# Kernel tuning notes

Measured on AMD Instinct MI355X. Metric: run time of the kernel, lower is better.

The kernel has to match this reference:

```python
import jax, jax.numpy as jnp
import numpy as np

_EPS = 1e-6

def _qmul(q1, q2):  # xyzw quaternion product
    x1, y1, z1, w1 = q1[..., 0], q1[..., 1], q1[..., 2], q1[..., 3]
    x2, y2, z2, w2 = q2[..., 0], q2[..., 1], q2[..., 2], q2[..., 3]
    return jnp.stack([
        w1 * x2 + x1 * w2 + y1 * z2 - z1 * y2,
        w1 * y2 + y1 * w2 + z1 * x2 - x1 * z2,
        w1 * z2 + z1 * w2 + x1 * y2 - y1 * x2,
        w1 * w2 - x1 * x2 - y1 * y2 - z1 * z2], axis=-1)

def _qrot(q, v):  # rotate v by unit quaternion q (xyzw)
    qv, qw = q[..., :3], q[..., 3:4]
    t = 2.0 * jnp.cross(qv, v)
    return v + qw * t + jnp.cross(qv, t)

def _so3_log(q):  # quaternion (xyzw) -> rotation vector phi
    qv, qw = q[..., :3], q[..., 3:4]
    n2 = jnp.sum(qv * qv, axis=-1, keepdims=True)
    small = n2 < _EPS * _EPS
    n = jnp.sqrt(jnp.where(small, 1.0, n2))
    factor = jnp.where(small,
                       2.0 / qw - (2.0 / 3.0) * n2 / qw ** 3,
                       2.0 * jnp.arctan2(n, qw) / n)
    return factor * qv

def _so3_exp(phi):  # rotation vector -> quaternion (xyzw)
    t2 = jnp.sum(phi * phi, axis=-1, keepdims=True)
    small = t2 < _EPS * _EPS
    theta = jnp.sqrt(jnp.where(small, 1.0, t2))
    half = 0.5 * theta
    s = jnp.where(small, 0.5 - t2 / 48.0, jnp.sin(half) / theta)
    w = jnp.where(small, 1.0 - t2 / 8.0, jnp.cos(half))
    return jnp.concatenate([s * phi, w], axis=-1)

def _jl(phi, v):  # SO3 left Jacobian J_l(phi) @ v
    t2 = jnp.sum(phi * phi, axis=-1, keepdims=True)
    small = t2 < _EPS * _EPS
    t2s = jnp.where(small, 1.0, t2)
    theta = jnp.sqrt(t2s)
    a = jnp.where(small, 0.5 - t2 / 24.0, (1.0 - jnp.cos(theta)) / t2s)
    b = jnp.where(small, 1.0 / 6.0 - t2 / 120.0, (theta - jnp.sin(theta)) / (t2s * theta))
    c1 = jnp.cross(phi, v)
    return v + a * c1 + b * jnp.cross(phi, c1)

def _jl_inv(phi, v):  # SO3 left Jacobian inverse J_l^{-1}(phi) @ v
    t2 = jnp.sum(phi * phi, axis=-1, keepdims=True)
    small = t2 < _EPS * _EPS
    t2s = jnp.where(small, 1.0, t2)
    theta = jnp.sqrt(t2s)
    s = jnp.sin(theta)
    s_safe = jnp.where(jnp.abs(s) < _EPS, _EPS, s)
    c = jnp.where(small, 1.0 / 12.0 + t2 / 720.0,
                  1.0 / t2s - (1.0 + jnp.cos(theta)) / (2.0 * theta * s_safe))
    c1 = jnp.cross(phi, v)
    return v - 0.5 * c1 + c * jnp.cross(phi, c1)

def _se3_inv(T):
    t, q = T[..., :3], T[..., 3:]
    qi = q * jnp.array([-1.0, -1.0, -1.0, 1.0], dtype=T.dtype)
    return jnp.concatenate([-_qrot(qi, t), qi], axis=-1)

def _se3_mul(T1, T2):
    t1, q1 = T1[..., :3], T1[..., 3:]
    t2, q2 = T2[..., :3], T2[..., 3:]
    return jnp.concatenate([t1 + _qrot(q1, t2), _qmul(q1, q2)], axis=-1)

def _se3_log(T):  # SE3 -> se3 [tau, phi]
    t, q = T[..., :3], T[..., 3:]
    phi = _so3_log(q)
    return jnp.concatenate([_jl_inv(phi, t), phi], axis=-1)

def _se3_exp(xi):  # se3 [tau, phi] -> SE3
    tau, phi = xi[..., :3], xi[..., 3:]
    q = _so3_exp(phi)
    return jnp.concatenate([_jl(phi, tau), q], axis=-1)

def _forward(input_poses, time):
    # duplicate first/last pose (inter_begin_and_end=True)
    poses = jnp.concatenate([input_poses[:, :1], input_poses, input_poses[:, -1:]], axis=1)
    B, P = poses.shape[0], poses.shape[1]
    S = P - 3  # number of spline segments
    u = time.reshape(-1)  # [K]
    K = u.shape[0]
    U = jnp.stack([jnp.ones_like(u), u, u * u, u * u * u], axis=0)  # [4,K]
    M = jnp.array([[5., 3., -3., 1.], [1., 3., 3., -2.], [0., 0., 0., 1.]], dtype=u.dtype) / 6.0
    w = M @ U  # [3,K] cumulative B-spline weights
    p0, p1 = poses[:, 0:S], poses[:, 1:S + 1]
    p2, p3 = poses[:, 2:S + 2], poses[:, 3:S + 3]
    d0 = _se3_log(_se3_mul(_se3_inv(p0), p1))  # [B,S,6]
    d1 = _se3_log(_se3_mul(_se3_inv(p1), p2))
    d2 = _se3_log(_se3_mul(_se3_inv(p2), p3))
    A0 = _se3_exp(d0[:, :, None, :] * w[0][None, None, :, None])  # [B,S,K,7]
    A1 = _se3_exp(d1[:, :, None, :] * w[1][None, None, :, None])
    A2 = _se3_exp(d2[:, :, None, :] * w[2][None, None, :, None])
    Td = jnp.broadcast_to(p0[:, :, None, :], (B, S, K, 7))
    out = _se3_mul(_se3_mul(_se3_mul(Td, A0), A1), A2)
    return out.reshape(B, S * K, 7)

def setup_inputs() -> dict:
    key = jax.random.key(0)
    k1, k2, k3 = jax.random.split(key, 3)
    B, N, K = 32, 2048, 32
    t = jax.random.normal(k1, (B, N, 3), dtype=jnp.float32) * 2.0
    q = jax.random.normal(k2, (B, N, 4), dtype=jnp.float32)
    q = q / jnp.linalg.norm(q, axis=-1, keepdims=True)
    q = jnp.where(q[..., 3:4] < 0, -q, q)  # qw >= 0 for well-conditioned Log
    input_poses = jnp.concatenate([t, q], axis=-1)
    time = jax.random.uniform(k3, (1, 1, K), dtype=jnp.float32)
    return {"input_poses": input_poses, "time": time}

def reference(input_poses, time):
    return _forward(input_poses, time)
```

## Files before the change

### kernel.cpp

```cpp
#include <hip/hip_runtime.h>
#include <cmath>

namespace {

constexpr int BATCH  = 32;
constexpr int NPOSE  = 2048;
constexpr int KSAMP  = 32;
constexpr int NSEG   = NPOSE - 1;
constexpr int NDELTA = NPOSE + 1;
constexpr int SEGB   = 32;
constexpr float EPS  = 1e-6f;
constexpr float EPS2 = 1e-12f;
constexpr float INV_TWO_PI = 0.15915494309189535f;

struct V3 { float x, y, z; };
struct Q4 { float x, y, z, w; };
struct SE3 { V3 t; Q4 q; };

__device__ __forceinline__ float frcp(float x)  { return __builtin_amdgcn_rcpf(x); }
__device__ __forceinline__ float fsqrt(float x) { return __builtin_amdgcn_sqrtf(x); }
__device__ __forceinline__ float fsin(float x)  { return __builtin_amdgcn_sinf(x * INV_TWO_PI); }
__device__ __forceinline__ float fcos(float x)  { return __builtin_amdgcn_cosf(x * INV_TWO_PI); }

__device__ __forceinline__ V3 v3add(V3 a, V3 b) { return {a.x + b.x, a.y + b.y, a.z + b.z}; }
__device__ __forceinline__ V3 v3sub(V3 a, V3 b) { return {a.x - b.x, a.y - b.y, a.z - b.z}; }
__device__ __forceinline__ V3 v3scl(V3 a, float s) { return {a.x * s, a.y * s, a.z * s}; }
__device__ __forceinline__ float v3dot(V3 a, V3 b) { return a.x * b.x + a.y * b.y + a.z * b.z; }
__device__ __forceinline__ V3 v3cross(V3 a, V3 b) {
    return {a.y * b.z - a.z * b.y, a.z * b.x - a.x * b.z, a.x * b.y - a.y * b.x};
}

__device__ __forceinline__ V3 qrot(Q4 q, V3 v) {
    V3 qv{q.x, q.y, q.z};
    V3 t = v3scl(v3cross(qv, v), 2.0f);
    return v3add(v3add(v, v3scl(t, q.w)), v3cross(qv, t));
}

__device__ __forceinline__ Q4 qmul(Q4 a, Q4 b) {
    return {a.w * b.x + a.x * b.w + a.y * b.z - a.z * b.y,
            a.w * b.y + a.y * b.w + a.z * b.x - a.x * b.z,
            a.w * b.z + a.z * b.w + a.x * b.y - a.y * b.x,
            a.w * b.w - a.x * b.x - a.y * b.y - a.z * b.z};
}

__device__ __forceinline__ SE3 se3_mul(SE3 A, SE3 Bv) {
    SE3 r;
    r.t = v3add(A.t, qrot(A.q, Bv.t));
    r.q = qmul(A.q, Bv.q);
    return r;
}

__device__ __forceinline__ float facos(float x) {
    float ax = fabsf(x);
    float p = -0.0012624911f;
    p = p * ax + 0.0066700901f;
    p = p * ax - 0.0170881256f;
    p = p * ax + 0.0308918810f;
    p = p * ax - 0.0501743046f;
    p = p * ax + 0.0889789874f;
    p = p * ax - 0.2145988016f;
    p = p * ax + 1.5707963050f;
    float r = fsqrt(fmaxf(1.0f - ax, 0.0f)) * p;
    return (x >= 0.0f) ? r : (3.14159265358979f - r);
}

__device__ __forceinline__ V3 so3_log(Q4 q) {
    V3 qv{q.x, q.y, q.z};
    float n2 = v3dot(qv, qv);
    bool small = n2 < EPS2;
    float n = fsqrt(small ? 1.0f : n2);
    float iw = frcp(q.w);
    float f_small = 2.0f * iw - (2.0f / 3.0f) * n2 * iw * iw * iw;
    float wc = fminf(fmaxf(q.w, -1.0f), 1.0f);
    float f_big = 2.0f * facos(wc) * frcp(n);
    return v3scl(qv, small ? f_small : f_big);
}

__device__ __forceinline__ V3 jl_inv(V3 phi, V3 v) {
    float t2 = v3dot(phi, phi);
    bool small = t2 < EPS2;
    float t2s = small ? 1.0f : t2;
    float theta = fsqrt(t2s);
    float s = fsin(theta), cth = fcos(theta);
    float s_safe = (fabsf(s) < EPS) ? EPS : s;
    float c_big = frcp(t2s) - (1.0f + cth) * frcp(2.0f * theta * s_safe);
    float c = small ? (1.0f / 12.0f + t2 * (1.0f / 720.0f)) : c_big;
    V3 c1 = v3cross(phi, v);
    return v3add(v3sub(v, v3scl(c1, 0.5f)), v3scl(v3cross(phi, c1), c));
}

__global__ __launch_bounds__(256) void lie_delta_kernel(
    const float* __restrict__ poses,
    float4* __restrict__ ws)
{
    const int i = blockIdx.x * 256 + threadIdx.x;
    const int b = blockIdx.y;
    if (i >= NDELTA) return;

    int ia = max(i - 1, 0);
    int ib = min(i, NPOSE - 1);
    const float* Pa = poses + ((size_t)b * NPOSE + ia) * 7;
    const float* Pb = poses + ((size_t)b * NPOSE + ib) * 7;
    V3 ta{Pa[0], Pa[1], Pa[2]}; Q4 qa{Pa[3], Pa[4], Pa[5], Pa[6]};
    V3 tb{Pb[0], Pb[1], Pb[2]}; Q4 qb{Pb[3], Pb[4], Pb[5], Pb[6]};

    Q4 qi{-qa.x, -qa.y, -qa.z, qa.w};
    V3 trel = qrot(qi, v3sub(tb, ta));
    Q4 qrel = qmul(qi, qb);
    V3 phi = so3_log(qrel);
    V3 tau = jl_inv(phi, trel);

    float n2 = v3dot(phi, phi);
    float nphi = fsqrt(n2);
    float inv_n = frcp(fmaxf(nphi, 1e-20f));
    V3 u  = v3scl(phi, inv_n);
    V3 c1 = v3cross(u, tau);
    V3 c2 = v3cross(u, c1);

    float4* row = ws + ((size_t)b * NDELTA + i) * 4;
    row[0] = make_float4(tau.x, tau.y, tau.z, nphi);
    row[1] = make_float4(u.x,  u.y,  u.z,  0.0f);
    row[2] = make_float4(c1.x, c1.y, c1.z, 0.0f);
    row[3] = make_float4(c2.x, c2.y, c2.z, 0.0f);
}

__device__ __forceinline__ SE3 exp_fast(float4 A, float4 U, float4 C1, float4 C2, float w) {
    float th = fmaxf(w * A.w, 1e-12f);
    float sh = fsin(0.5f * th), ch = fcos(0.5f * th);
    float it = frcp(th);
    float sA = 2.0f * sh * sh * it;
    float sB = 1.0f - 2.0f * sh * ch * it;
    SE3 r;
    r.q = {sh * U.x, sh * U.y, sh * U.z, ch};
    r.t = {w * (A.x + sA * C1.x + sB * C2.x),
           w * (A.y + sA * C1.y + sB * C2.y),
           w * (A.z + sA * C1.z + sB * C2.z)};
    return r;
}

__global__ __launch_bounds__(256) void lie_spline_kernel(
    const float* __restrict__ poses,
    const float* __restrict__ timev,
    const float4* __restrict__ ws,
    float* __restrict__ out)
{
    __shared__ float4 sdel[(SEGB + 2) * 5];
    __shared__ __align__(16) float stage[SEGB * KSAMP * 7];

    const int b   = blockIdx.y;
    const int s0  = blockIdx.x * SEGB;
    const int tid = threadIdx.x;

    if (tid < (SEGB + 2) * 4) {
        int row = tid >> 2, r = tid & 3;
        int idx = min(s0 + row, NDELTA - 1);
        sdel[row * 5 + r] = ws[((size_t)b * NDELTA + idx) * 4 + r];
    }

    const int segl = tid >> 3;
    const int s    = s0 + segl;
    const int m    = tid & 7;

    int ip = min(max(s - 1, 0), NPOSE - 1);
    const float* P0 = poses + ((size_t)b * NPOSE + ip) * 7;
    const SE3 Tp{{P0[0], P0[1], P0[2]}, {P0[3], P0[4], P0[5], P0[6]}};
    float4 uvec = reinterpret_cast<const float4*>(timev)[m];

    __syncthreads();

    const float4* R = sdel + segl * 5;
    float4 A0 = R[0],  U0 = R[1],  C10 = R[2],  C20 = R[3];
    float4 A1 = R[5],  U1 = R[6],  C11 = R[7],  C21 = R[8];
    float4 A2 = R[10], U2 = R[11], C12 = R[12], C22 = R[13];

    __align__(16) float buf[28];
    const float us[4] = {uvec.x, uvec.y, uvec.z, uvec.w};
    #pragma unroll
    for (int j = 0; j < 4; ++j) {
        float u  = us[j];
        float u2 = u * u, u3 = u2 * u;
        const float c6 = 1.0f / 6.0f;
        float w0 = (5.0f + 3.0f * u - 3.0f * u2 + u3) * c6;
        float w1 = (1.0f + 3.0f * u + 3.0f * u2 - 2.0f * u3) * c6;
        float w2 = u3 * c6;
        SE3 T = se3_mul(Tp, exp_fast(A0, U0, C10, C20, w0));
        T = se3_mul(T, exp_fast(A1, U1, C11, C21, w1));
        T = se3_mul(T, exp_fast(A2, U2, C12, C22, w2));
        float* d = buf + j * 7;
        d[0] = T.t.x; d[1] = T.t.y; d[2] = T.t.z;
        d[3] = T.q.x; d[4] = T.q.y; d[5] = T.q.z; d[6] = T.q.w;
    }

    if (s < NSEG) {
        float4* sv = reinterpret_cast<float4*>(stage + segl * (KSAMP * 7) + m * 28);
        const float4* bv = reinterpret_cast<const float4*>(buf);
        #pragma unroll
        for (int c = 0; c < 7; ++c) sv[c] = bv[c];
    }
    __syncthreads();

    int nseg_blk = min(NSEG - s0, SEGB);
    int nvec = nseg_blk * (KSAMP * 7 / 4);
    const float4* svv = reinterpret_cast<const float4*>(stage);
    float4* ov = reinterpret_cast<float4*>(out + ((size_t)b * NSEG + s0) * (size_t)(KSAMP * 7));
    for (int j = tid; j < nvec; j += 256) ov[j] = svv[j];
}

}

extern "C" void kernel_launch(void* const* d_in, const int* in_sizes, int n_in,
                              void* d_out, int out_size, void* d_ws, size_t ws_size,
                              hipStream_t stream) {
    const float* poses = (const float*)d_in[0];
    const float* timev = (const float*)d_in[1];
    float* out = (float*)d_out;
    float4* ws = (float4*)d_ws;
    (void)in_sizes; (void)n_in; (void)out_size; (void)ws_size;

    dim3 g1((NDELTA + 255) / 256, BATCH);
    lie_delta_kernel<<<g1, 256, 0, stream>>>(poses, ws);

    dim3 g2((NSEG + SEGB - 1) / SEGB, BATCH);
    lie_spline_kernel<<<g2, 256, 0, stream>>>(poses, timev, ws, out);
}
```

Measured before the change: 90.02 us.

## Fuse delta computation into spline kernel, computing deltas in shared memory per block

Removes the separate delta kernel and its global workspace round trip. Each spline block now computes its 34 needed deltas (SE3 log plus precomputed cross terms) directly into shared memory, with the first 34 threads doing the work before the barrier. It also skips pose evaluation for out-of-range segments and writes the staged poses straight from registers instead of through a private buffer. In exchange, one launch is saved, but each block recomputes two boundary deltas and serializes the transcendental-heavy delta work on a subset of threads before the barrier.

```diff
diff --git a/kernel.cpp b/kernel.cpp
--- a/kernel.cpp
+++ b/kernel.cpp
@@ -89,41 +89,6 @@
     return v3add(v3sub(v, v3scl(c1, 0.5f)), v3scl(v3cross(phi, c1), c));
 }
 
-__global__ __launch_bounds__(256) void lie_delta_kernel(
-    const float* __restrict__ poses,
-    float4* __restrict__ ws)
-{
-    const int i = blockIdx.x * 256 + threadIdx.x;
-    const int b = blockIdx.y;
-    if (i >= NDELTA) return;
-
-    int ia = max(i - 1, 0);
-    int ib = min(i, NPOSE - 1);
-    const float* Pa = poses + ((size_t)b * NPOSE + ia) * 7;
-    const float* Pb = poses + ((size_t)b * NPOSE + ib) * 7;
-    V3 ta{Pa[0], Pa[1], Pa[2]}; Q4 qa{Pa[3], Pa[4], Pa[5], Pa[6]};
-    V3 tb{Pb[0], Pb[1], Pb[2]}; Q4 qb{Pb[3], Pb[4], Pb[5], Pb[6]};
-
-    Q4 qi{-qa.x, -qa.y, -qa.z, qa.w};
-    V3 trel = qrot(qi, v3sub(tb, ta));
-    Q4 qrel = qmul(qi, qb);
-    V3 phi = so3_log(qrel);
-    V3 tau = jl_inv(phi, trel);
-
-    float n2 = v3dot(phi, phi);
-    float nphi = fsqrt(n2);
-    float inv_n = frcp(fmaxf(nphi, 1e-20f));
-    V3 u  = v3scl(phi, inv_n);
-    V3 c1 = v3cross(u, tau);
-    V3 c2 = v3cross(u, c1);
-
-    float4* row = ws + ((size_t)b * NDELTA + i) * 4;
-    row[0] = make_float4(tau.x, tau.y, tau.z, nphi);
-    row[1] = make_float4(u.x,  u.y,  u.z,  0.0f);
-    row[2] = make_float4(c1.x, c1.y, c1.z, 0.0f);
-    row[3] = make_float4(c2.x, c2.y, c2.z, 0.0f);
-}
-
 __device__ __forceinline__ SE3 exp_fast(float4 A, float4 U, float4 C1, float4 C2, float w) {
     float th = fmaxf(w * A.w, 1e-12f);
     float sh = fsin(0.5f * th), ch = fcos(0.5f * th);
@@ -138,10 +103,9 @@
     return r;
 }
 
-__global__ __launch_bounds__(256) void lie_spline_kernel(
+__global__ __launch_bounds__(256) void lie_spline_fused(
     const float* __restrict__ poses,
     const float* __restrict__ timev,
-    const float4* __restrict__ ws,
     float* __restrict__ out)
 {
     __shared__ float4 sdel[(SEGB + 2) * 5];
@@ -151,51 +115,78 @@
     const int s0  = blockIdx.x * SEGB;
     const int tid = threadIdx.x;
 
-    if (tid < (SEGB + 2) * 4) {
-        int row = tid >> 2, r = tid & 3;
-        int idx = min(s0 + row, NDELTA - 1);
-        sdel[row * 5 + r] = ws[((size_t)b * NDELTA + idx) * 4 + r];
-    }
-
     const int segl = tid >> 3;
+    const int m    = tid & 7;
     const int s    = s0 + segl;
-    const int m    = tid & 7;
 
     int ip = min(max(s - 1, 0), NPOSE - 1);
     const float* P0 = poses + ((size_t)b * NPOSE + ip) * 7;
     const SE3 Tp{{P0[0], P0[1], P0[2]}, {P0[3], P0[4], P0[5], P0[6]}};
-    float4 uvec = reinterpret_cast<const float4*>(timev)[m];
-
+    const float4 uvec = reinterpret_cast<const float4*>(timev)[m];
+
+    if (tid < SEGB + 2) {
+        int i = min(s0 + tid, NDELTA - 1);
+        int ia = max(i - 1, 0);
+        int ib = min(i, NPOSE - 1);
+        const float* Pa = poses + ((size_t)b * NPOSE + ia) * 7;
+        const float* Pb = poses + ((size_t)b * NPOSE + ib) * 7;
+        V3 ta{Pa[0], Pa[1], Pa[2]}; Q4 qa{Pa[3], Pa[4], Pa[5], Pa[6]};
+        V3 tb{Pb[0], Pb[1], Pb[2]}; Q4 qb{Pb[3], Pb[4], Pb[5], Pb[6]};
+
+        Q4 qi{-qa.x, -qa.y, -qa.z, qa.w};
+        V3 trel = qrot(qi, v3sub(tb, ta));
+        Q4 qrel = qmul(qi, qb);
+        V3 phi = so3_log(qrel);
+        V3 tau = jl_inv(phi, trel);
+
+        float nphi = fsqrt(v3dot(phi, phi));
+        float inv_n = frcp(fmaxf(nphi, 1e-20f));
+        V3 u  = v3scl(phi, inv_n);
+        V3 c1 = v3cross(u, tau);
+        V3 c2 = v3cross(u, c1);
+
+        float4* r = sdel + tid * 5;
+        r[0] = make_float4(tau.x, tau.y, tau.z, nphi);
+        r[1] = make_float4(u.x,  u.y,  u.z,  0.0f);
+        r[2] = make_float4(c1.x, c1.y, c1.z, 0.0f);
+        r[3] = make_float4(c2.x, c2.y, c2.z, 0.0f);
+    }
     __syncthreads();
 
-    const float4* R = sdel + segl * 5;
-    float4 A0 = R[0],  U0 = R[1],  C10 = R[2],  C20 = R[3];
-    float4 A1 = R[5],  U1 = R[6],  C11 = R[7],  C21 = R[8];
-    float4 A2 = R[10], U2 = R[11], C12 = R[12], C22 = R[13];
-
-    __align__(16) float buf[28];
-    const float us[4] = {uvec.x, uvec.y, uvec.z, uvec.w};
-    #pragma unroll
-    for (int j = 0; j < 4; ++j) {
-        float u  = us[j];
-        float u2 = u * u, u3 = u2 * u;
+    if (s < NSEG) {
+        const float4* R = sdel + segl * 5;
+        const float4 A0 = R[0],  U0 = R[1],  C10 = R[2],  C20 = R[3];
+        const float4 A1 = R[5],  U1 = R[6],  C11 = R[7],  C21 = R[8];
+        const float4 A2 = R[10], U2 = R[11], C12 = R[12], C22 = R[13];
+
         const float c6 = 1.0f / 6.0f;
-        float w0 = (5.0f + 3.0f * u - 3.0f * u2 + u3) * c6;
-        float w1 = (1.0f + 3.0f * u + 3.0f * u2 - 2.0f * u3) * c6;
-        float w2 = u3 * c6;
-        SE3 T = se3_mul(Tp, exp_fast(A0, U0, C10, C20, w0));
-        T = se3_mul(T, exp_fast(A1, U1, C11, C21, w1));
-        T = se3_mul(T, exp_fast(A2, U2, C12, C22, w2));
-        float* d = buf + j * 7;
-        d[0] = T.t.x; d[1] = T.t.y; d[2] = T.t.z;
-        d[3] = T.q.x; d[4] = T.q.y; d[5] = T.q.z; d[6] = T.q.w;
-    }
-
-    if (s < NSEG) {
+        SE3 T0, T1, T2, T3;
+        #define POSE_AT(u_, Tdst_)                                              \
+        {                                                                       \
+            float u = (u_);                                                     \
+            float u2 = u * u, u3 = u2 * u;                                      \
+            float w0 = (5.0f + 3.0f * u - 3.0f * u2 + u3) * c6;                 \
+            float w1 = (1.0f + 3.0f * u + 3.0f * u2 - 2.0f * u3) * c6;          \
+            float w2 = u3 * c6;                                                 \
+            SE3 T = se3_mul(Tp, exp_fast(A0, U0, C10, C20, w0));                \
+            T = se3_mul(T, exp_fast(A1, U1, C11, C21, w1));                     \
+            T = se3_mul(T, exp_fast(A2, U2, C12, C22, w2));                     \
+            Tdst_ = T;                                                          \
+        }
+        POSE_AT(uvec.x, T0)
+        POSE_AT(uvec.y, T1)
+        POSE_AT(uvec.z, T2)
+        POSE_AT(uvec.w, T3)
+        #undef POSE_AT
+
         float4* sv = reinterpret_cast<float4*>(stage + segl * (KSAMP * 7) + m * 28);
-        const float4* bv = reinterpret_cast<const float4*>(buf);
-        #pragma unroll
-        for (int c = 0; c < 7; ++c) sv[c] = bv[c];
+        sv[0] = make_float4(T0.t.x, T0.t.y, T0.t.z, T0.q.x);
+        sv[1] = make_float4(T0.q.y, T0.q.z, T0.q.w, T1.t.x);
+        sv[2] = make_float4(T1.t.y, T1.t.z, T1.q.x, T1.q.y);
+        sv[3] = make_float4(T1.q.z, T1.q.w, T2.t.x, T2.t.y);
+        sv[4] = make_float4(T2.t.z, T2.q.x, T2.q.y, T2.q.z);
+        sv[5] = make_float4(T2.q.w, T3.t.x, T3.t.y, T3.t.z);
+        sv[6] = make_float4(T3.q.x, T3.q.y, T3.q.z, T3.q.w);
     }
     __syncthreads();
 
@@ -214,12 +205,8 @@
     const float* poses = (const float*)d_in[0];
     const float* timev = (const float*)d_in[1];
     float* out = (float*)d_out;
-    float4* ws = (float4*)d_ws;
-    (void)in_sizes; (void)n_in; (void)out_size; (void)ws_size;
-
-    dim3 g1((NDELTA + 255) / 256, BATCH);
-    lie_delta_kernel<<<g1, 256, 0, stream>>>(poses, ws);
-
-    dim3 g2((NSEG + SEGB - 1) / SEGB, BATCH);
-    lie_spline_kernel<<<g2, 256, 0, stream>>>(poses, timev, ws, out);
-}
+    (void)in_sizes; (void)n_in; (void)out_size; (void)d_ws; (void)ws_size;
+
+    dim3 grid((NSEG + SEGB - 1) / SEGB, BATCH);
+    lie_spline_fused<<<grid, 256, 0, stream>>>(poses, timev, out);
+}
```

Result: faster. 87.47 us (-2.8%).
